# Performance work log

Hardware: AMD Instinct MI355X
Metric: run time of the kernel (lower is better)

The kernel has to match this reference:

```python
import jax, jax.numpy as jnp
import numpy as np

H, HD = 8, 32            # num_heads, head_dim
OUT = H * HD             # out_channels = 256
NUM_GRAPHS = 1


def segment_softmax(logits, seg, num_segments):
    m = jax.ops.segment_max(logits, seg, num_segments=num_segments)
    m = jnp.where(jnp.isfinite(m), m, 0.0)
    e = jnp.exp(logits - m[seg])
    s = jax.ops.segment_sum(e, seg, num_segments=num_segments)
    return e / (s[seg] + 1e-16)


def setup_inputs():
    key = jax.random.key(0)
    ks = jax.random.split(key, 16)
    N, E, IN = 30000, 600000, 128
    s = 0.05
    return {
        "x": jax.random.normal(ks[0], (N, IN), jnp.float32),
        "edge_index": jax.random.randint(ks[1], (2, E), 0, N, jnp.int32),
        "edge_attr": jax.random.normal(ks[2], (E,), jnp.float32),
        "batch": jnp.zeros((N,), jnp.int32),
        # per-head GATConv params (stacked over heads)
        "W": jax.random.normal(ks[3], (H, IN, HD), jnp.float32) * s,
        "a_src": jax.random.normal(ks[4], (H, HD), jnp.float32) * s,
        "a_dst": jax.random.normal(ks[5], (H, HD), jnp.float32) * s,
        "conv_b": jnp.zeros((H, HD), jnp.float32),
        # shared fc (used twice in forward)
        "fc_w": jax.random.normal(ks[6], (OUT, OUT), jnp.float32) * s,
        "fc_b": jnp.zeros((OUT,), jnp.float32),
        "ln_w": jnp.ones((OUT,), jnp.float32),
        "ln_b": jnp.zeros((OUT,), jnp.float32),
        "gate_w": jax.random.normal(ks[7], (1, OUT), jnp.float32) * s,
        "gate_b": jnp.zeros((1,), jnp.float32),
        "gfc_w": jax.random.normal(ks[8], (OUT, OUT), jnp.float32) * s,
        "gfc_b": jnp.zeros((OUT,), jnp.float32),
    }


def reference(x, edge_index, edge_attr, batch, W, a_src, a_dst, conv_b,
              fc_w, fc_b, ln_w, ln_b, gate_w, gate_b, gfc_w, gfc_b):
    N = x.shape[0]
    # (dropout p=0.2 is identity in eval mode)
    # --- multi-head GATConv (heads=1 each, vectorized over H); PyG default
    # add_self_loops=True; edge_dim=None so edge_attr is ignored by the conv.
    loops = jnp.arange(N, dtype=edge_index.dtype)
    src = jnp.concatenate([edge_index[0], loops])  # [Etot]
    dst = jnp.concatenate([edge_index[1], loops])
    xp = jnp.einsum('ni,hid->nhd', x, W)                    # [N,H,HD]
    alpha_src = jnp.sum(xp * a_src[None], axis=-1)          # [N,H]
    alpha_dst = jnp.sum(xp * a_dst[None], axis=-1)          # [N,H]
    logits = jax.nn.leaky_relu(alpha_src[src] + alpha_dst[dst], 0.2)  # [Etot,H]
    alpha = segment_softmax(logits, dst, N)                 # [Etot,H]
    msg = alpha[:, :, None] * xp[src]                        # [Etot,H,HD]
    out = jax.ops.segment_sum(msg, dst, num_segments=N) + conv_b[None]
    x_local = out.reshape(N, OUT)                            # concat over heads
    # --- dense re-attention / softmax fusion
    sa = jax.nn.softmax(jax.nn.leaky_relu(x_local @ fc_w.T + fc_b, 0.01), axis=-1)
    x_local = jax.nn.leaky_relu(x_local * sa, 0.2)
    x_local = x_local @ fc_w.T + fc_b
    # LayerNorm (eps=1e-5)
    mu = jnp.mean(x_local, axis=-1, keepdims=True)
    var = jnp.mean(jnp.square(x_local - mu), axis=-1, keepdims=True)
    x_local = (x_local - mu) / jnp.sqrt(var + 1e-5) * ln_w + ln_b
    # F.normalize(p=2, dim=1)
    nrm = jnp.sqrt(jnp.sum(jnp.square(x_local), axis=1, keepdims=True))
    x_local = x_local / jnp.maximum(nrm, 1e-12)
    # --- GlobalAttention pooling
    gate = (x_local @ gate_w.T + gate_b)[:, 0]               # [N]
    g = segment_softmax(gate, batch, NUM_GRAPHS)             # [N]
    x_global = jax.ops.segment_sum(g[:, None] * x_local, batch,
                                   num_segments=NUM_GRAPHS)  # [1,OUT]
    ga = jax.nn.softmax(jax.nn.relu(x_global @ gfc_w.T + gfc_b), axis=-1)
    return x_local * ga[batch]                               # [N,OUT]
```

## Files before the change

kernel.cpp:

```cpp
#include <hip/hip_runtime.h>


#define PAD 64
#define CSTR 16

typedef __attribute__((ext_vector_type(8))) short bf16x8;
typedef __attribute__((ext_vector_type(4))) float f32x4;

__device__ __forceinline__ float leaky_f(float v, float s) { return v > 0.f ? v : s * v; }
__device__ __forceinline__ unsigned short f2bf(float f) {
  unsigned int u = __float_as_uint(f);
  u += 0x7fffu + ((u >> 16) & 1u);
  return (unsigned short)(u >> 16);
}
__device__ __forceinline__ float bf2f(unsigned short u) {
  return __uint_as_float(((unsigned int)u) << 16);
}
__device__ __forceinline__ float bf_lo(unsigned int u) {
  return __uint_as_float(u << 16);
}
__device__ __forceinline__ float bf_hi(unsigned int u) {
  return __uint_as_float(u & 0xffff0000u);
}
__device__ __forceinline__ float red16_sum(float v) {
#pragma unroll
  for (int m = 1; m < 16; m <<= 1) v += __shfl_xor(v, m);
  return v;
}
__device__ __forceinline__ float red16_max(float v) {
#pragma unroll
  for (int m = 1; m < 16; m <<= 1) v = fmaxf(v, __shfl_xor(v, m));
  return v;
}

__global__ void repack_zero_kernel(const float* __restrict__ W, const float* __restrict__ fc_w,
                                   const float* __restrict__ gfc_w,
                                   unsigned short* __restrict__ Wb,
                                   unsigned short* __restrict__ fcB, float* __restrict__ gfcT,
                                   int* __restrict__ count, int n) {
  int i = blockIdx.x * 256 + threadIdx.x;
  if (i < 256 * 128) {
    int c = i >> 7, k = i & 127;
    Wb[i] = f2bf(W[((c >> 5) * 128 + k) * 32 + (c & 31)]);
  } else if (i < 256 * 128 + 256 * 256) {
    int j = i - 256 * 128;
    fcB[j] = f2bf(fc_w[j]);
  } else if (i < 256 * 128 + 2 * 256 * 256) {
    int j = i - 256 * 128 - 256 * 256;
    gfcT[j] = gfc_w[(j & 255) * 256 + (j >> 8)];
  }
  if (i < n) count[i * CSTR] = 0;
}

__device__ __forceinline__ void gemm_body_f32(
    const float* __restrict__ A, const unsigned short* __restrict__ B,
    int row0, int n_rows, int K, short As[64][72], short Bs[256][72],
    f32x4 acc[4][4]) {
  int t = threadIdx.x;
  int wave = t >> 6, lane = t & 63;
  int m16 = lane & 15, quad = lane >> 4;
  int wc = wave * 64;
  for (int k0 = 0; k0 < K; k0 += 64) {
#pragma unroll
    for (int p = 0; p < 4; ++p) {
      int e = (p * 256 + t) * 4;
      int row = e >> 6, k = e & 63;
      int ar = row0 + row; if (ar > n_rows - 1) ar = n_rows - 1;
      float4 q = *(const float4*)(A + (size_t)ar * K + k0 + k);
      unsigned int lo = (unsigned int)f2bf(q.x) | ((unsigned int)f2bf(q.y) << 16);
      unsigned int hi = (unsigned int)f2bf(q.z) | ((unsigned int)f2bf(q.w) << 16);
      *(uint2*)&As[row][k] = make_uint2(lo, hi);
    }
#pragma unroll
    for (int p = 0; p < 8; ++p) {
      int e = (p * 256 + t) * 8;
      int nn = e >> 6, k = e & 63;
      uint4 q = *(const uint4*)(B + (size_t)nn * K + k0 + k);
      *(uint4*)&Bs[nn][k] = q;
    }
    __syncthreads();
#pragma unroll
    for (int ks = 0; ks < 64; ks += 32) {
      bf16x8 af[4], bfr[4];
#pragma unroll
      for (int i = 0; i < 4; ++i)
        af[i] = *(const bf16x8*)&As[i * 16 + m16][ks + quad * 8];
#pragma unroll
      for (int j = 0; j < 4; ++j)
        bfr[j] = *(const bf16x8*)&Bs[wc + j * 16 + m16][ks + quad * 8];
#pragma unroll
      for (int i = 0; i < 4; ++i)
#pragma unroll
        for (int j = 0; j < 4; ++j)
          acc[i][j] = __builtin_amdgcn_mfma_f32_16x16x32_bf16(af[i], bfr[j], acc[i][j], 0, 0, 0);
    }
    __syncthreads();
  }
}

__global__ __launch_bounds__(256) void gemm_xp_scatter(
    const float* __restrict__ A, const unsigned short* __restrict__ B,
    const float* __restrict__ a_src, const float* __restrict__ a_dst,
    unsigned short* __restrict__ xpb, float* __restrict__ asrc,
    float* __restrict__ adst, int n_rows,
    const int* __restrict__ esrc, const int* __restrict__ edst,
    int* __restrict__ count, unsigned short* __restrict__ ssrc, int E,
    int scat_blocks) {
  __shared__ short As[64][72];
  __shared__ short Bs[256][72];
  if ((int)blockIdx.x < scat_blocks) {
    int base = ((int)blockIdx.x * 256 + threadIdx.x) * 4;
    if (base + 4 <= E) {
      int4 d4 = *(const int4*)(edst + base);
      int4 s4 = *(const int4*)(esrc + base);
      int p0 = atomicAdd(&count[d4.x * CSTR], 1);
      int p1 = atomicAdd(&count[d4.y * CSTR], 1);
      int p2 = atomicAdd(&count[d4.z * CSTR], 1);
      int p3 = atomicAdd(&count[d4.w * CSTR], 1);
      if (p0 < PAD) ssrc[(size_t)d4.x * PAD + p0] = (unsigned short)s4.x;
      if (p1 < PAD) ssrc[(size_t)d4.y * PAD + p1] = (unsigned short)s4.y;
      if (p2 < PAD) ssrc[(size_t)d4.z * PAD + p2] = (unsigned short)s4.z;
      if (p3 < PAD) ssrc[(size_t)d4.w * PAD + p3] = (unsigned short)s4.w;
    } else {
      for (int i = base; i < E; ++i) {
        int d = edst[i];
        int p = atomicAdd(&count[d * CSTR], 1);
        if (p < PAD) ssrc[(size_t)d * PAD + p] = (unsigned short)esrc[i];
      }
    }
    return;
  }
  int t = threadIdx.x;
  int wave = t >> 6, lane = t & 63;
  int m16 = lane & 15, quad = lane >> 4;
  int wc = wave * 64;
  int row0 = ((int)blockIdx.x - scat_blocks) * 64;
  f32x4 acc[4][4];
#pragma unroll
  for (int i = 0; i < 4; ++i)
#pragma unroll
    for (int j = 0; j < 4; ++j) acc[i][j] = (f32x4){0.f, 0.f, 0.f, 0.f};
  gemm_body_f32(A, B, row0, n_rows, 128, As, Bs, acc);

  float av[4], bd[4];
#pragma unroll
  for (int j = 0; j < 4; ++j) {
    int c = wc + j * 16 + m16;
    av[j] = a_src[c];
    bd[j] = a_dst[c];
  }
#pragma unroll
  for (int i = 0; i < 4; ++i)
#pragma unroll
    for (int v = 0; v < 4; ++v) {
      int r = row0 + i * 16 + quad * 4 + v;
      if (r < n_rows) {
#pragma unroll
        for (int j = 0; j < 4; ++j)
          xpb[(size_t)r * 256 + wc + j * 16 + m16] = f2bf(acc[i][j][v]);
      }
      float s0 = acc[i][0][v] * av[0] + acc[i][1][v] * av[1];
      float s1 = acc[i][2][v] * av[2] + acc[i][3][v] * av[3];
      float d0 = acc[i][0][v] * bd[0] + acc[i][1][v] * bd[1];
      float d1 = acc[i][2][v] * bd[2] + acc[i][3][v] * bd[3];
      s0 = red16_sum(s0); s1 = red16_sum(s1);
      d0 = red16_sum(d0); d1 = red16_sum(d1);
      if (m16 == 0 && r < n_rows) {
        asrc[(size_t)r * 8 + 2 * wave] = s0;
        asrc[(size_t)r * 8 + 2 * wave + 1] = s1;
        adst[(size_t)r * 8 + 2 * wave] = d0;
        adst[(size_t)r * 8 + 2 * wave + 1] = d1;
      }
    }
}

__global__ __launch_bounds__(256) void agg_kernel(
    const unsigned short* __restrict__ xpb, const float* __restrict__ asrc,
    const float* __restrict__ adst, const int* __restrict__ count,
    const unsigned short* __restrict__ ssrc, const float* __restrict__ conv_b,
    unsigned short* __restrict__ xlocb, int n_nodes) {
  int t = threadIdx.x;
  int lane = t & 63;
  int hl = lane & 31;
  int half = lane >> 5;
  int wv = t >> 6;
  int n = blockIdx.x * 8 + wv * 2 + half;
  bool active = n < n_nodes;
  int nn = active ? n : 0;
  int hc = hl >> 2;
  int hp = hl & 7;
  int up = hl >> 3;
  int srcbase = (half << 5) + hc;

  float ad_p = adst[nn * 8 + hp];
  float ad_c = adst[nn * 8 + hc];

  float p = __expf(leaky_f(asrc[nn * 8 + hc] + ad_c, 0.2f));
  uint4 q = *(const uint4*)(xpb + (size_t)nn * 256 + hl * 8);
  float acc[8];
  acc[0] = p * bf_lo(q.x); acc[1] = p * bf_hi(q.x);
  acc[2] = p * bf_lo(q.y); acc[3] = p * bf_hi(q.y);
  acc[4] = p * bf_lo(q.z); acc[5] = p * bf_hi(q.z);
  acc[6] = p * bf_lo(q.w); acc[7] = p * bf_hi(q.w);
  float ssum = p;

  int beg = nn * PAD;
  int end = beg + (active ? count[nn * CSTR] : 0);
  int j = beg;
  for (; j + 4 <= end; j += 4) {
    ushort4 s4 = *(const ushort4*)(ssrc + j);
    int svp = (up & 1) ? ((up & 2) ? s4.w : s4.y) : ((up & 2) ? s4.z : s4.x);
    float pp = __expf(leaky_f(asrc[svp * 8 + hp] + ad_p, 0.2f));
    uint4 q0 = *(const uint4*)(xpb + (size_t)s4.x * 256 + hl * 8);
    uint4 q1 = *(const uint4*)(xpb + (size_t)s4.y * 256 + hl * 8);
    uint4 q2 = *(const uint4*)(xpb + (size_t)s4.z * 256 + hl * 8);
    uint4 q3 = *(const uint4*)(xpb + (size_t)s4.w * 256 + hl * 8);
    float p0 = __shfl(pp, srcbase);
    float p1 = __shfl(pp, srcbase + 8);
    float p2 = __shfl(pp, srcbase + 16);
    float p3 = __shfl(pp, srcbase + 24);
    acc[0] += p0 * bf_lo(q0.x); acc[1] += p0 * bf_hi(q0.x);
    acc[2] += p0 * bf_lo(q0.y); acc[3] += p0 * bf_hi(q0.y);
    acc[4] += p0 * bf_lo(q0.z); acc[5] += p0 * bf_hi(q0.z);
    acc[6] += p0 * bf_lo(q0.w); acc[7] += p0 * bf_hi(q0.w);
    acc[0] += p1 * bf_lo(q1.x); acc[1] += p1 * bf_hi(q1.x);
    acc[2] += p1 * bf_lo(q1.y); acc[3] += p1 * bf_hi(q1.y);
    acc[4] += p1 * bf_lo(q1.z); acc[5] += p1 * bf_hi(q1.z);
    acc[6] += p1 * bf_lo(q1.w); acc[7] += p1 * bf_hi(q1.w);
    acc[0] += p2 * bf_lo(q2.x); acc[1] += p2 * bf_hi(q2.x);
    acc[2] += p2 * bf_lo(q2.y); acc[3] += p2 * bf_hi(q2.y);
    acc[4] += p2 * bf_lo(q2.z); acc[5] += p2 * bf_hi(q2.z);
    acc[6] += p2 * bf_lo(q2.w); acc[7] += p2 * bf_hi(q2.w);
    acc[0] += p3 * bf_lo(q3.x); acc[1] += p3 * bf_hi(q3.x);
    acc[2] += p3 * bf_lo(q3.y); acc[3] += p3 * bf_hi(q3.y);
    acc[4] += p3 * bf_lo(q3.z); acc[5] += p3 * bf_hi(q3.z);
    acc[6] += p3 * bf_lo(q3.w); acc[7] += p3 * bf_hi(q3.w);
    ssum += p0 + p1 + p2 + p3;
  }
  for (; j < end; ++j) {
    int sv = ssrc[j];
    float p1 = __expf(leaky_f(asrc[sv * 8 + hc] + ad_c, 0.2f));
    uint4 q1 = *(const uint4*)(xpb + (size_t)sv * 256 + hl * 8);
    acc[0] += p1 * bf_lo(q1.x); acc[1] += p1 * bf_hi(q1.x);
    acc[2] += p1 * bf_lo(q1.y); acc[3] += p1 * bf_hi(q1.y);
    acc[4] += p1 * bf_lo(q1.z); acc[5] += p1 * bf_hi(q1.z);
    acc[6] += p1 * bf_lo(q1.w); acc[7] += p1 * bf_hi(q1.w);
    ssum += p1;
  }
  if (!active) return;
  float inv = 1.f / (ssum + 1e-16f);
  float4 b0 = *(const float4*)(conv_b + hl * 8);
  float4 b1 = *(const float4*)(conv_b + hl * 8 + 4);
  unsigned int w0 = (unsigned int)f2bf(acc[0] * inv + b0.x) |
                    ((unsigned int)f2bf(acc[1] * inv + b0.y) << 16);
  unsigned int w1 = (unsigned int)f2bf(acc[2] * inv + b0.z) |
                    ((unsigned int)f2bf(acc[3] * inv + b0.w) << 16);
  unsigned int w2 = (unsigned int)f2bf(acc[4] * inv + b1.x) |
                    ((unsigned int)f2bf(acc[5] * inv + b1.y) << 16);
  unsigned int w3 = (unsigned int)f2bf(acc[6] * inv + b1.z) |
                    ((unsigned int)f2bf(acc[7] * inv + b1.w) << 16);
  *(uint4*)(xlocb + (size_t)n * 256 + hl * 8) = make_uint4(w0, w1, w2, w3);
}

__global__ __launch_bounds__(256) void gemm_sm_ln(
    const unsigned short* __restrict__ A, const unsigned short* __restrict__ B,
    const float* __restrict__ bias, const float* __restrict__ ln_w,
    const float* __restrict__ ln_b, const float* __restrict__ gate_w,
    const float* __restrict__ gate_b, unsigned short* __restrict__ Cout,
    float* __restrict__ pooled, float* __restrict__ pooledS, int n_rows) {
  __shared__ short X2[64][264];
  __shared__ short Bs[256][72];
  __shared__ float red[4][64];
  __shared__ float rowv[64];
  __shared__ float eg[64];
  int t = threadIdx.x;
  int wave = t >> 6, lane = t & 63;
  int m16 = lane & 15, quad = lane >> 4;
  int wc = wave * 64;
  int row0 = blockIdx.x * 64;

#pragma unroll
  for (int p = 0; p < 8; ++p) {
    int e = (p * 256 + t) * 8;
    int row = e >> 8, col = e & 255;
    int ar = row0 + row; if (ar > n_rows - 1) ar = n_rows - 1;
    uint4 qv = *(const uint4*)(A + (size_t)ar * 256 + col);
    *(uint4*)&X2[row][col] = qv;
  }

  f32x4 acc[4][4];
#pragma unroll
  for (int i = 0; i < 4; ++i)
#pragma unroll
    for (int j = 0; j < 4; ++j) acc[i][j] = (f32x4){0.f, 0.f, 0.f, 0.f};

  for (int k0 = 0; k0 < 256; k0 += 64) {
#pragma unroll
    for (int p = 0; p < 8; ++p) {
      int e = (p * 256 + t) * 8;
      int nn = e >> 6, k = e & 63;
      uint4 qv = *(const uint4*)(B + (size_t)nn * 256 + k0 + k);
      *(uint4*)&Bs[nn][k] = qv;
    }
    __syncthreads();
#pragma unroll
    for (int ks = 0; ks < 64; ks += 32) {
      bf16x8 af[4], bfr[4];
#pragma unroll
      for (int i = 0; i < 4; ++i)
        af[i] = *(const bf16x8*)&X2[i * 16 + m16][k0 + ks + quad * 8];
#pragma unroll
      for (int j = 0; j < 4; ++j)
        bfr[j] = *(const bf16x8*)&Bs[wc + j * 16 + m16][ks + quad * 8];
#pragma unroll
      for (int i = 0; i < 4; ++i)
#pragma unroll
        for (int j = 0; j < 4; ++j)
          acc[i][j] = __builtin_amdgcn_mfma_f32_16x16x32_bf16(af[i], bfr[j], acc[i][j], 0, 0, 0);
    }
    __syncthreads();
  }

  float bvv[4];
#pragma unroll
  for (int j = 0; j < 4; ++j) bvv[j] = bias[wc + j * 16 + m16];
#pragma unroll
  for (int i = 0; i < 4; ++i)
#pragma unroll
    for (int j = 0; j < 4; ++j)
#pragma unroll
      for (int v = 0; v < 4; ++v)
        acc[i][j][v] = leaky_f(acc[i][j][v] + bvv[j], 0.01f);

  float M[4][4];
#pragma unroll
  for (int i = 0; i < 4; ++i)
#pragma unroll
    for (int v = 0; v < 4; ++v) {
      float m = fmaxf(fmaxf(acc[i][0][v], acc[i][1][v]), fmaxf(acc[i][2][v], acc[i][3][v]));
      M[i][v] = red16_max(m);
    }
  if (m16 == 0)
#pragma unroll
    for (int i = 0; i < 4; ++i)
#pragma unroll
      for (int v = 0; v < 4; ++v) red[wave][i * 16 + quad * 4 + v] = M[i][v];
  __syncthreads();
  if (t < 64) rowv[t] = fmaxf(fmaxf(red[0][t], red[1][t]), fmaxf(red[2][t], red[3][t]));
  __syncthreads();
#pragma unroll
  for (int i = 0; i < 4; ++i)
#pragma unroll
    for (int v = 0; v < 4; ++v) M[i][v] = rowv[i * 16 + quad * 4 + v];
  __syncthreads();

  float S[4][4];
#pragma unroll
  for (int i = 0; i < 4; ++i)
#pragma unroll
    for (int v = 0; v < 4; ++v) {
#pragma unroll
      for (int j = 0; j < 4; ++j) acc[i][j][v] = __expf(acc[i][j][v] - M[i][v]);
      float s = acc[i][0][v] + acc[i][1][v] + acc[i][2][v] + acc[i][3][v];
      S[i][v] = red16_sum(s);
    }
  if (m16 == 0)
#pragma unroll
    for (int i = 0; i < 4; ++i)
#pragma unroll
      for (int v = 0; v < 4; ++v) red[wave][i * 16 + quad * 4 + v] = S[i][v];
  __syncthreads();
  if (t < 64) rowv[t] = red[0][t] + red[1][t] + red[2][t] + red[3][t];
  __syncthreads();

#pragma unroll
  for (int i = 0; i < 4; ++i)
#pragma unroll
    for (int v = 0; v < 4; ++v) {
      int rl = i * 16 + quad * 4 + v;
      float inv = 1.f / rowv[rl];
#pragma unroll
      for (int j = 0; j < 4; ++j) {
        int c = wc + j * 16 + m16;
        float xv = bf2f((unsigned short)X2[rl][c]);
        X2[rl][c] = (short)f2bf(leaky_f(xv * acc[i][j][v] * inv, 0.2f));
      }
    }

#pragma unroll
  for (int i = 0; i < 4; ++i)
#pragma unroll
    for (int j = 0; j < 4; ++j) acc[i][j] = (f32x4){0.f, 0.f, 0.f, 0.f};
  for (int k0 = 0; k0 < 256; k0 += 64) {
#pragma unroll
    for (int p = 0; p < 8; ++p) {
      int e = (p * 256 + t) * 8;
      int nn = e >> 6, k = e & 63;
      uint4 qv = *(const uint4*)(B + (size_t)nn * 256 + k0 + k);
      *(uint4*)&Bs[nn][k] = qv;
    }
    __syncthreads();
#pragma unroll
    for (int ks = 0; ks < 64; ks += 32) {
      bf16x8 af[4], bfr[4];
#pragma unroll
      for (int i = 0; i < 4; ++i)
        af[i] = *(const bf16x8*)&X2[i * 16 + m16][k0 + ks + quad * 8];
#pragma unroll
      for (int j = 0; j < 4; ++j)
        bfr[j] = *(const bf16x8*)&Bs[wc + j * 16 + m16][ks + quad * 8];
#pragma unroll
      for (int i = 0; i < 4; ++i)
#pragma unroll
        for (int j = 0; j < 4; ++j)
          acc[i][j] = __builtin_amdgcn_mfma_f32_16x16x32_bf16(af[i], bfr[j], acc[i][j], 0, 0, 0);
    }
    __syncthreads();
  }

  float lw[4], lb[4], gw[4];
#pragma unroll
  for (int j = 0; j < 4; ++j) {
    int c = wc + j * 16 + m16;
    bvv[j] = bias[c]; lw[j] = ln_w[c]; lb[j] = ln_b[c]; gw[j] = gate_w[c];
  }
#pragma unroll
  for (int i = 0; i < 4; ++i)
#pragma unroll
    for (int j = 0; j < 4; ++j)
#pragma unroll
      for (int v = 0; v < 4; ++v) acc[i][j][v] += bvv[j];

  float MU[4][4];
#pragma unroll
  for (int i = 0; i < 4; ++i)
#pragma unroll
    for (int v = 0; v < 4; ++v)
      MU[i][v] = red16_sum(acc[i][0][v] + acc[i][1][v] + acc[i][2][v] + acc[i][3][v]);
  if (m16 == 0)
#pragma unroll
    for (int i = 0; i < 4; ++i)
#pragma unroll
      for (int v = 0; v < 4; ++v) red[wave][i * 16 + quad * 4 + v] = MU[i][v];
  __syncthreads();
  if (t < 64) rowv[t] = (red[0][t] + red[1][t] + red[2][t] + red[3][t]) * (1.f / 256.f);
  __syncthreads();
#pragma unroll
  for (int i = 0; i < 4; ++i)
#pragma unroll
    for (int v = 0; v < 4; ++v) MU[i][v] = rowv[i * 16 + quad * 4 + v];
  __syncthreads();
#pragma unroll
  for (int i = 0; i < 4; ++i)
#pragma unroll
    for (int j = 0; j < 4; ++j)
#pragma unroll
      for (int v = 0; v < 4; ++v) acc[i][j][v] -= MU[i][v];

  float RS[4][4];
#pragma unroll
  for (int i = 0; i < 4; ++i)
#pragma unroll
    for (int v = 0; v < 4; ++v) {
      float qq = acc[i][0][v] * acc[i][0][v] + acc[i][1][v] * acc[i][1][v] +
                 acc[i][2][v] * acc[i][2][v] + acc[i][3][v] * acc[i][3][v];
      RS[i][v] = red16_sum(qq);
    }
  if (m16 == 0)
#pragma unroll
    for (int i = 0; i < 4; ++i)
#pragma unroll
      for (int v = 0; v < 4; ++v) red[wave][i * 16 + quad * 4 + v] = RS[i][v];
  __syncthreads();
  if (t < 64)
    rowv[t] = rsqrtf((red[0][t] + red[1][t] + red[2][t] + red[3][t]) * (1.f / 256.f) + 1e-5f);
  __syncthreads();
#pragma unroll
  for (int i = 0; i < 4; ++i)
#pragma unroll
    for (int v = 0; v < 4; ++v) RS[i][v] = rowv[i * 16 + quad * 4 + v];
  __syncthreads();
#pragma unroll
  for (int i = 0; i < 4; ++i)
#pragma unroll
    for (int j = 0; j < 4; ++j)
#pragma unroll
      for (int v = 0; v < 4; ++v)
        acc[i][j][v] = acc[i][j][v] * RS[i][v] * lw[j] + lb[j];

  float NV[4][4];
#pragma unroll
  for (int i = 0; i < 4; ++i)
#pragma unroll
    for (int v = 0; v < 4; ++v) {
      float qq = acc[i][0][v] * acc[i][0][v] + acc[i][1][v] * acc[i][1][v] +
                 acc[i][2][v] * acc[i][2][v] + acc[i][3][v] * acc[i][3][v];
      NV[i][v] = red16_sum(qq);
    }
  if (m16 == 0)
#pragma unroll
    for (int i = 0; i < 4; ++i)
#pragma unroll
      for (int v = 0; v < 4; ++v) red[wave][i * 16 + quad * 4 + v] = NV[i][v];
  __syncthreads();
  if (t < 64)
    rowv[t] = 1.f / fmaxf(sqrtf(red[0][t] + red[1][t] + red[2][t] + red[3][t]), 1e-12f);
  __syncthreads();
#pragma unroll
  for (int i = 0; i < 4; ++i)
#pragma unroll
    for (int v = 0; v < 4; ++v) NV[i][v] = rowv[i * 16 + quad * 4 + v];
  __syncthreads();
#pragma unroll
  for (int i = 0; i < 4; ++i)
#pragma unroll
    for (int j = 0; j < 4; ++j)
#pragma unroll
      for (int v = 0; v < 4; ++v) acc[i][j][v] *= NV[i][v];

  float GP[4][4];
#pragma unroll
  for (int i = 0; i < 4; ++i)
#pragma unroll
    for (int v = 0; v < 4; ++v) {
      float g = acc[i][0][v] * gw[0] + acc[i][1][v] * gw[1] +
                acc[i][2][v] * gw[2] + acc[i][3][v] * gw[3];
      GP[i][v] = red16_sum(g);
    }
  if (m16 == 0)
#pragma unroll
    for (int i = 0; i < 4; ++i)
#pragma unroll
      for (int v = 0; v < 4; ++v) red[wave][i * 16 + quad * 4 + v] = GP[i][v];
  __syncthreads();
  if (t < 64) {
    float gp = red[0][t] + red[1][t] + red[2][t] + red[3][t];
    float e = (row0 + t < n_rows) ? __expf(gp + gate_b[0]) : 0.f;
    eg[t] = e;
#pragma unroll
    for (int m = 1; m < 64; m <<= 1) e += __shfl_xor(e, m);
    if (t == 0) pooledS[blockIdx.x] = e;
  }
  __syncthreads();

  {
    float pt[4] = {0.f, 0.f, 0.f, 0.f};
#pragma unroll
    for (int i = 0; i < 4; ++i)
#pragma unroll
      for (int v = 0; v < 4; ++v) {
        float w = eg[i * 16 + quad * 4 + v];
#pragma unroll
        for (int j = 0; j < 4; ++j) pt[j] += w * acc[i][j][v];
      }
#pragma unroll
    for (int j = 0; j < 4; ++j) {
      float sj = pt[j];
      sj += __shfl_xor(sj, 16);
      sj += __shfl_xor(sj, 32);
      if (quad == 0) pooled[(size_t)blockIdx.x * 256 + wc + j * 16 + m16] = sj;
    }
  }

#pragma unroll
  for (int i = 0; i < 4; ++i)
#pragma unroll
    for (int v = 0; v < 4; ++v) {
      int r = row0 + i * 16 + quad * 4 + v;
      if (r < n_rows) {
#pragma unroll
        for (int j = 0; j < 4; ++j)
          Cout[(size_t)r * 256 + wc + j * 16 + m16] = f2bf(acc[i][j][v]);
      }
    }
}

__global__ __launch_bounds__(1024) void finalize_gfc(
    const float* __restrict__ pooled, const float* __restrict__ pooledS, int nb,
    const float* __restrict__ gfcT, const float* __restrict__ gfc_b,
    float* __restrict__ ga) {
  __shared__ float sm[1024];
  __shared__ float xs[256];
  __shared__ float av[256];
  int t = threadIdx.x, c = t & 255, part = t >> 8;
  float s = 0.f;
  for (int b = t; b < nb; b += 1024) s += pooledS[b];
  sm[t] = s;
  __syncthreads();
  for (int st = 512; st > 0; st >>= 1) {
    if (t < st) sm[t] += sm[t + st];
    __syncthreads();
  }
  float S = sm[0];
  __syncthreads();
  float xc = 0.f;
#pragma unroll 4
  for (int b = part; b < nb; b += 4) xc += pooled[(size_t)b * 256 + c];
  sm[t] = xc;
  __syncthreads();
  if (part == 0) xs[c] = (sm[c] + sm[c + 256] + sm[c + 512] + sm[c + 768]) / (S + 1e-16f);
  __syncthreads();
  float a = 0.f;
  for (int i = part * 64; i < part * 64 + 64; ++i) a += xs[i] * gfcT[i * 256 + c];
  sm[t] = a;
  __syncthreads();
  if (part == 0)
    av[c] = fmaxf(sm[c] + sm[c + 256] + sm[c + 512] + sm[c + 768] + gfc_b[c], 0.f);
  __syncthreads();
  sm[t] = (t < 256) ? av[t] : -1e30f;
  __syncthreads();
  for (int st = 512; st > 0; st >>= 1) {
    if (t < st) sm[t] = fmaxf(sm[t], sm[t + st]);
    __syncthreads();
  }
  float m = sm[0];
  __syncthreads();
  if (part == 0) av[c] = __expf(av[c] - m);
  __syncthreads();
  sm[t] = (t < 256) ? av[t] : 0.f;
  __syncthreads();
  for (int st = 512; st > 0; st >>= 1) {
    if (t < st) sm[t] += sm[t + st];
    __syncthreads();
  }
  if (part == 0) ga[c] = av[c] / sm[0];
}

__global__ void out_kernel(const ushort4* __restrict__ xlb4, const float4* __restrict__ ga4,
                           float4* __restrict__ out4, int total4) {
  int i = blockIdx.x * 256 + threadIdx.x;
  if (i >= total4) return;
  ushort4 q = xlb4[i];
  float4 g = ga4[i & 63];
  float4 v;
  v.x = bf2f(q.x) * g.x; v.y = bf2f(q.y) * g.y;
  v.z = bf2f(q.z) * g.z; v.w = bf2f(q.w) * g.w;
  out4[i] = v;
}

extern "C" void kernel_launch(void* const* d_in, const int* in_sizes, int n_in,
                              void* d_out, int out_size, void* d_ws, size_t ws_size,
                              hipStream_t stream) {
  const float* x      = (const float*)d_in[0];
  const int* edge_idx = (const int*)d_in[1];
  const float* W      = (const float*)d_in[4];
  const float* a_src  = (const float*)d_in[5];
  const float* a_dst  = (const float*)d_in[6];
  const float* conv_b = (const float*)d_in[7];
  const float* fc_w   = (const float*)d_in[8];
  const float* fc_b   = (const float*)d_in[9];
  const float* ln_w   = (const float*)d_in[10];
  const float* ln_b   = (const float*)d_in[11];
  const float* gate_w = (const float*)d_in[12];
  const float* gate_b = (const float*)d_in[13];
  const float* gfc_w  = (const float*)d_in[14];
  const float* gfc_b  = (const float*)d_in[15];
  (void)n_in; (void)out_size; (void)ws_size;

  int N = in_sizes[0] / 128;
  int E = in_sizes[1] / 2;
  const int* src = edge_idx;
  const int* dst = edge_idx + E;

  char* p = (char*)d_ws;
  auto alloc = [&](size_t bytes) -> char* {
    char* r = p;
    p += (bytes + 255) & ~(size_t)255;
    return r;
  };
  int g64 = (N + 63) / 64;
  unsigned short* xlocb = (unsigned short*)alloc((size_t)N * 256 * 2);
  unsigned short* xpb  = (unsigned short*)alloc((size_t)N * 256 * 2);
  unsigned short* xlb  = (unsigned short*)alloc((size_t)N * 256 * 2);
  float* asrc  = (float*)alloc((size_t)N * 8 * 4);
  float* adst  = (float*)alloc((size_t)N * 8 * 4);
  unsigned short* Wb   = (unsigned short*)alloc(256 * 128 * 2);
  unsigned short* fcB  = (unsigned short*)alloc(256 * 256 * 2);
  float* gfcT  = (float*)alloc(256 * 256 * 4);
  int*   count = (int*)alloc((size_t)N * CSTR * 4);
  unsigned short* ssrc = (unsigned short*)alloc((size_t)N * PAD * 2);
  float* pooled  = (float*)alloc((size_t)g64 * 256 * 4);
  float* pooledS = (float*)alloc((size_t)g64 * 4);
  float* ga    = (float*)alloc(1024);

  int eb4 = (E + 1023) / 1024;

  repack_zero_kernel<<<(256 * 128 + 2 * 256 * 256 + 255) / 256, 256, 0, stream>>>(
      W, fc_w, gfc_w, Wb, fcB, gfcT, count, N);
  gemm_xp_scatter<<<eb4 + g64, 256, 0, stream>>>(
      x, Wb, a_src, a_dst, xpb, asrc, adst, N, src, dst, count, ssrc, E, eb4);
  agg_kernel<<<(N + 7) / 8, 256, 0, stream>>>(
      xpb, asrc, adst, count, ssrc, conv_b, xlocb, N);
  gemm_sm_ln<<<g64, 256, 0, stream>>>(xlocb, fcB, fc_b, ln_w, ln_b, gate_w,
                                      gate_b, xlb, pooled, pooledS, N);
  finalize_gfc<<<1, 1024, 0, stream>>>(pooled, pooledS, g64, gfcT, gfc_b, ga);
  out_kernel<<<(N * 64 + 255) / 256, 256, 0, stream>>>(
      (const ushort4*)xlb, (const float4*)ga, (float4*)d_out, N * 64);
}
```

Measured before the change: 242.6 us.

## Fuse aggregation into fc GEMM and merge finalize with output scaling via flag

The edge-aggregation kernel is folded into the fc/softmax/LayerNorm GEMM kernel, so each 64-row block gathers its neighbours straight into shared memory instead of writing and re-reading an intermediate bf16 buffer. The single-block gfc finalize and the elementwise output kernel become one grid-stride kernel. In it, block 0 computes the gate vector and sets a flag, and the other blocks spin on that flag before scaling. This removes two launches and one round trip of N×256 data through global memory. The trade-off is far fewer blocks for the gather phase (one per 64 rows instead of one per 8), which may hurt latency hiding. The spin-wait also relies on block 0 being scheduled.

Result: slower. 958.3 us (+295.0%).

```diff
diff --git a/kernel.cpp b/kernel.cpp
--- a/kernel.cpp
+++ b/kernel.cpp
@@ -37,7 +37,7 @@
                                    const float* __restrict__ gfc_w,
                                    unsigned short* __restrict__ Wb,
                                    unsigned short* __restrict__ fcB, float* __restrict__ gfcT,
-                                   int* __restrict__ count, int n) {
+                                   int* __restrict__ count, int* __restrict__ flag, int n) {
   int i = blockIdx.x * 256 + threadIdx.x;
   if (i < 256 * 128) {
     int c = i >> 7, k = i & 127;
@@ -50,6 +50,7 @@
     gfcT[j] = gfc_w[(j & 255) * 256 + (j >> 8)];
   }
   if (i < n) count[i * CSTR] = 0;
+  if (i == 0) flag[0] = 0;
 }
 
 __device__ __forceinline__ void gemm_body_f32(
@@ -174,96 +175,11 @@
     }
 }
 
-__global__ __launch_bounds__(256) void agg_kernel(
+__global__ __launch_bounds__(256) void agg_sm_ln(
     const unsigned short* __restrict__ xpb, const float* __restrict__ asrc,
     const float* __restrict__ adst, const int* __restrict__ count,
     const unsigned short* __restrict__ ssrc, const float* __restrict__ conv_b,
-    unsigned short* __restrict__ xlocb, int n_nodes) {
-  int t = threadIdx.x;
-  int lane = t & 63;
-  int hl = lane & 31;
-  int half = lane >> 5;
-  int wv = t >> 6;
-  int n = blockIdx.x * 8 + wv * 2 + half;
-  bool active = n < n_nodes;
-  int nn = active ? n : 0;
-  int hc = hl >> 2;
-  int hp = hl & 7;
-  int up = hl >> 3;
-  int srcbase = (half << 5) + hc;
-
-  float ad_p = adst[nn * 8 + hp];
-  float ad_c = adst[nn * 8 + hc];
-
-  float p = __expf(leaky_f(asrc[nn * 8 + hc] + ad_c, 0.2f));
-  uint4 q = *(const uint4*)(xpb + (size_t)nn * 256 + hl * 8);
-  float acc[8];
-  acc[0] = p * bf_lo(q.x); acc[1] = p * bf_hi(q.x);
-  acc[2] = p * bf_lo(q.y); acc[3] = p * bf_hi(q.y);
-  acc[4] = p * bf_lo(q.z); acc[5] = p * bf_hi(q.z);
-  acc[6] = p * bf_lo(q.w); acc[7] = p * bf_hi(q.w);
-  float ssum = p;
-
-  int beg = nn * PAD;
-  int end = beg + (active ? count[nn * CSTR] : 0);
-  int j = beg;
-  for (; j + 4 <= end; j += 4) {
-    ushort4 s4 = *(const ushort4*)(ssrc + j);
-    int svp = (up & 1) ? ((up & 2) ? s4.w : s4.y) : ((up & 2) ? s4.z : s4.x);
-    float pp = __expf(leaky_f(asrc[svp * 8 + hp] + ad_p, 0.2f));
-    uint4 q0 = *(const uint4*)(xpb + (size_t)s4.x * 256 + hl * 8);
-    uint4 q1 = *(const uint4*)(xpb + (size_t)s4.y * 256 + hl * 8);
-    uint4 q2 = *(const uint4*)(xpb + (size_t)s4.z * 256 + hl * 8);
-    uint4 q3 = *(const uint4*)(xpb + (size_t)s4.w * 256 + hl * 8);
-    float p0 = __shfl(pp, srcbase);
-    float p1 = __shfl(pp, srcbase + 8);
-    float p2 = __shfl(pp, srcbase + 16);
-    float p3 = __shfl(pp, srcbase + 24);
-    acc[0] += p0 * bf_lo(q0.x); acc[1] += p0 * bf_hi(q0.x);
-    acc[2] += p0 * bf_lo(q0.y); acc[3] += p0 * bf_hi(q0.y);
-    acc[4] += p0 * bf_lo(q0.z); acc[5] += p0 * bf_hi(q0.z);
-    acc[6] += p0 * bf_lo(q0.w); acc[7] += p0 * bf_hi(q0.w);
-    acc[0] += p1 * bf_lo(q1.x); acc[1] += p1 * bf_hi(q1.x);
-    acc[2] += p1 * bf_lo(q1.y); acc[3] += p1 * bf_hi(q1.y);
-    acc[4] += p1 * bf_lo(q1.z); acc[5] += p1 * bf_hi(q1.z);
-    acc[6] += p1 * bf_lo(q1.w); acc[7] += p1 * bf_hi(q1.w);
-    acc[0] += p2 * bf_lo(q2.x); acc[1] += p2 * bf_hi(q2.x);
-    acc[2] += p2 * bf_lo(q2.y); acc[3] += p2 * bf_hi(q2.y);
-    acc[4] += p2 * bf_lo(q2.z); acc[5] += p2 * bf_hi(q2.z);
-    acc[6] += p2 * bf_lo(q2.w); acc[7] += p2 * bf_hi(q2.w);
-    acc[0] += p3 * bf_lo(q3.x); acc[1] += p3 * bf_hi(q3.x);
-    acc[2] += p3 * bf_lo(q3.y); acc[3] += p3 * bf_hi(q3.y);
-    acc[4] += p3 * bf_lo(q3.z); acc[5] += p3 * bf_hi(q3.z);
-    acc[6] += p3 * bf_lo(q3.w); acc[7] += p3 * bf_hi(q3.w);
-    ssum += p0 + p1 + p2 + p3;
-  }
-  for (; j < end; ++j) {
-    int sv = ssrc[j];
-    float p1 = __expf(leaky_f(asrc[sv * 8 + hc] + ad_c, 0.2f));
-    uint4 q1 = *(const uint4*)(xpb + (size_t)sv * 256 + hl * 8);
-    acc[0] += p1 * bf_lo(q1.x); acc[1] += p1 * bf_hi(q1.x);
-    acc[2] += p1 * bf_lo(q1.y); acc[3] += p1 * bf_hi(q1.y);
-    acc[4] += p1 * bf_lo(q1.z); acc[5] += p1 * bf_hi(q1.z);
-    acc[6] += p1 * bf_lo(q1.w); acc[7] += p1 * bf_hi(q1.w);
-    ssum += p1;
-  }
-  if (!active) return;
-  float inv = 1.f / (ssum + 1e-16f);
-  float4 b0 = *(const float4*)(conv_b + hl * 8);
-  float4 b1 = *(const float4*)(conv_b + hl * 8 + 4);
-  unsigned int w0 = (unsigned int)f2bf(acc[0] * inv + b0.x) |
-                    ((unsigned int)f2bf(acc[1] * inv + b0.y) << 16);
-  unsigned int w1 = (unsigned int)f2bf(acc[2] * inv + b0.z) |
-                    ((unsigned int)f2bf(acc[3] * inv + b0.w) << 16);
-  unsigned int w2 = (unsigned int)f2bf(acc[4] * inv + b1.x) |
-                    ((unsigned int)f2bf(acc[5] * inv + b1.y) << 16);
-  unsigned int w3 = (unsigned int)f2bf(acc[6] * inv + b1.z) |
-                    ((unsigned int)f2bf(acc[7] * inv + b1.w) << 16);
-  *(uint4*)(xlocb + (size_t)n * 256 + hl * 8) = make_uint4(w0, w1, w2, w3);
-}
-
-__global__ __launch_bounds__(256) void gemm_sm_ln(
-    const unsigned short* __restrict__ A, const unsigned short* __restrict__ B,
+    const unsigned short* __restrict__ B,
     const float* __restrict__ bias, const float* __restrict__ ln_w,
     const float* __restrict__ ln_b, const float* __restrict__ gate_w,
     const float* __restrict__ gate_b, unsigned short* __restrict__ Cout,
@@ -279,14 +195,89 @@
   int wc = wave * 64;
   int row0 = blockIdx.x * 64;
 
-#pragma unroll
-  for (int p = 0; p < 8; ++p) {
-    int e = (p * 256 + t) * 8;
-    int row = e >> 8, col = e & 255;
-    int ar = row0 + row; if (ar > n_rows - 1) ar = n_rows - 1;
-    uint4 qv = *(const uint4*)(A + (size_t)ar * 256 + col);
-    *(uint4*)&X2[row][col] = qv;
-  }
+  {
+    int hl = lane & 31;
+    int half = lane >> 5;
+    int hc = hl >> 2;
+    int hp = hl & 7;
+    int up = hl >> 3;
+    int srcbase = (half << 5) + hc;
+    for (int it = 0; it < 8; ++it) {
+      int lr = wave * 16 + it * 2 + half;
+      int n = row0 + lr;
+      bool active = n < n_rows;
+      int nn = active ? n : 0;
+      float ad_p = adst[nn * 8 + hp];
+      float ad_c = adst[nn * 8 + hc];
+      float p = __expf(leaky_f(asrc[nn * 8 + hc] + ad_c, 0.2f));
+      uint4 q = *(const uint4*)(xpb + (size_t)nn * 256 + hl * 8);
+      float a8[8];
+      a8[0] = p * bf_lo(q.x); a8[1] = p * bf_hi(q.x);
+      a8[2] = p * bf_lo(q.y); a8[3] = p * bf_hi(q.y);
+      a8[4] = p * bf_lo(q.z); a8[5] = p * bf_hi(q.z);
+      a8[6] = p * bf_lo(q.w); a8[7] = p * bf_hi(q.w);
+      float ssum = p;
+      int beg = nn * PAD;
+      int end = beg + (active ? count[nn * CSTR] : 0);
+      int j = beg;
+      for (; j + 4 <= end; j += 4) {
+        ushort4 s4 = *(const ushort4*)(ssrc + j);
+        int svp = (up & 1) ? ((up & 2) ? s4.w : s4.y) : ((up & 2) ? s4.z : s4.x);
+        float pp = __expf(leaky_f(asrc[svp * 8 + hp] + ad_p, 0.2f));
+        uint4 q0 = *(const uint4*)(xpb + (size_t)s4.x * 256 + hl * 8);
+        uint4 q1 = *(const uint4*)(xpb + (size_t)s4.y * 256 + hl * 8);
+        uint4 q2 = *(const uint4*)(xpb + (size_t)s4.z * 256 + hl * 8);
+        uint4 q3 = *(const uint4*)(xpb + (size_t)s4.w * 256 + hl * 8);
+        float p0 = __shfl(pp, srcbase);
+        float p1 = __shfl(pp, srcbase + 8);
+        float p2 = __shfl(pp, srcbase + 16);
+        float p3 = __shfl(pp, srcbase + 24);
+        a8[0] += p0 * bf_lo(q0.x); a8[1] += p0 * bf_hi(q0.x);
+        a8[2] += p0 * bf_lo(q0.y); a8[3] += p0 * bf_hi(q0.y);
+        a8[4] += p0 * bf_lo(q0.z); a8[5] += p0 * bf_hi(q0.z);
+        a8[6] += p0 * bf_lo(q0.w); a8[7] += p0 * bf_hi(q0.w);
+        a8[0] += p1 * bf_lo(q1.x); a8[1] += p1 * bf_hi(q1.x);
+        a8[2] += p1 * bf_lo(q1.y); a8[3] += p1 * bf_hi(q1.y);
+        a8[4] += p1 * bf_lo(q1.z); a8[5] += p1 * bf_hi(q1.z);
+        a8[6] += p1 * bf_lo(q1.w); a8[7] += p1 * bf_hi(q1.w);
+        a8[0] += p2 * bf_lo(q2.x); a8[1] += p2 * bf_hi(q2.x);
+        a8[2] += p2 * bf_lo(q2.y); a8[3] += p2 * bf_hi(q2.y);
+        a8[4] += p2 * bf_lo(q2.z); a8[5] += p2 * bf_hi(q2.z);
+        a8[6] += p2 * bf_lo(q2.w); a8[7] += p2 * bf_hi(q2.w);
+        a8[0] += p3 * bf_lo(q3.x); a8[1] += p3 * bf_hi(q3.x);
+        a8[2] += p3 * bf_lo(q3.y); a8[3] += p3 * bf_hi(q3.y);
+        a8[4] += p3 * bf_lo(q3.z); a8[5] += p3 * bf_hi(q3.z);
+        a8[6] += p3 * bf_lo(q3.w); a8[7] += p3 * bf_hi(q3.w);
+        ssum += p0 + p1 + p2 + p3;
+      }
+      for (; j < end; ++j) {
+        int sv = ssrc[j];
+        float p1 = __expf(leaky_f(asrc[sv * 8 + hc] + ad_c, 0.2f));
+        uint4 q1 = *(const uint4*)(xpb + (size_t)sv * 256 + hl * 8);
+        a8[0] += p1 * bf_lo(q1.x); a8[1] += p1 * bf_hi(q1.x);
+        a8[2] += p1 * bf_lo(q1.y); a8[3] += p1 * bf_hi(q1.y);
+        a8[4] += p1 * bf_lo(q1.z); a8[5] += p1 * bf_hi(q1.z);
+        a8[6] += p1 * bf_lo(q1.w); a8[7] += p1 * bf_hi(q1.w);
+        ssum += p1;
+      }
+      unsigned int w0 = 0, w1 = 0, w2 = 0, w3 = 0;
+      if (active) {
+        float inv = 1.f / (ssum + 1e-16f);
+        float4 b0 = *(const float4*)(conv_b + hl * 8);
+        float4 b1 = *(const float4*)(conv_b + hl * 8 + 4);
+        w0 = (unsigned int)f2bf(a8[0] * inv + b0.x) |
+             ((unsigned int)f2bf(a8[1] * inv + b0.y) << 16);
+        w1 = (unsigned int)f2bf(a8[2] * inv + b0.z) |
+             ((unsigned int)f2bf(a8[3] * inv + b0.w) << 16);
+        w2 = (unsigned int)f2bf(a8[4] * inv + b1.x) |
+             ((unsigned int)f2bf(a8[5] * inv + b1.y) << 16);
+        w3 = (unsigned int)f2bf(a8[6] * inv + b1.z) |
+             ((unsigned int)f2bf(a8[7] * inv + b1.w) << 16);
+      }
+      *(uint4*)&X2[lr][hl * 8] = make_uint4(w0, w1, w2, w3);
+    }
+  }
+  __syncthreads();
 
   f32x4 acc[4][4];
 #pragma unroll
@@ -575,67 +566,67 @@
     }
 }
 
-__global__ __launch_bounds__(1024) void finalize_gfc(
+__global__ __launch_bounds__(256) void finalize_out(
     const float* __restrict__ pooled, const float* __restrict__ pooledS, int nb,
     const float* __restrict__ gfcT, const float* __restrict__ gfc_b,
-    float* __restrict__ ga) {
-  __shared__ float sm[1024];
+    const ushort4* __restrict__ xlb4, float4* __restrict__ out4, int total4,
+    float* __restrict__ gaBuf, int* __restrict__ flag) {
+  int t = threadIdx.x;
   __shared__ float xs[256];
-  __shared__ float av[256];
-  int t = threadIdx.x, c = t & 255, part = t >> 8;
-  float s = 0.f;
-  for (int b = t; b < nb; b += 1024) s += pooledS[b];
-  sm[t] = s;
-  __syncthreads();
-  for (int st = 512; st > 0; st >>= 1) {
-    if (t < st) sm[t] += sm[t + st];
-    __syncthreads();
-  }
-  float S = sm[0];
-  __syncthreads();
-  float xc = 0.f;
-#pragma unroll 4
-  for (int b = part; b < nb; b += 4) xc += pooled[(size_t)b * 256 + c];
-  sm[t] = xc;
-  __syncthreads();
-  if (part == 0) xs[c] = (sm[c] + sm[c + 256] + sm[c + 512] + sm[c + 768]) / (S + 1e-16f);
-  __syncthreads();
-  float a = 0.f;
-  for (int i = part * 64; i < part * 64 + 64; ++i) a += xs[i] * gfcT[i * 256 + c];
-  sm[t] = a;
-  __syncthreads();
-  if (part == 0)
-    av[c] = fmaxf(sm[c] + sm[c + 256] + sm[c + 512] + sm[c + 768] + gfc_b[c], 0.f);
-  __syncthreads();
-  sm[t] = (t < 256) ? av[t] : -1e30f;
-  __syncthreads();
-  for (int st = 512; st > 0; st >>= 1) {
-    if (t < st) sm[t] = fmaxf(sm[t], sm[t + st]);
-    __syncthreads();
-  }
-  float m = sm[0];
-  __syncthreads();
-  if (part == 0) av[c] = __expf(av[c] - m);
-  __syncthreads();
-  sm[t] = (t < 256) ? av[t] : 0.f;
-  __syncthreads();
-  for (int st = 512; st > 0; st >>= 1) {
-    if (t < st) sm[t] += sm[t + st];
-    __syncthreads();
-  }
-  if (part == 0) ga[c] = av[c] / sm[0];
-}
-
-__global__ void out_kernel(const ushort4* __restrict__ xlb4, const float4* __restrict__ ga4,
-                           float4* __restrict__ out4, int total4) {
-  int i = blockIdx.x * 256 + threadIdx.x;
-  if (i >= total4) return;
-  ushort4 q = xlb4[i];
-  float4 g = ga4[i & 63];
-  float4 v;
-  v.x = bf2f(q.x) * g.x; v.y = bf2f(q.y) * g.y;
-  v.z = bf2f(q.z) * g.z; v.w = bf2f(q.w) * g.w;
-  out4[i] = v;
+  __shared__ float red[256];
+  if (blockIdx.x == 0) {
+    float s = 0.f;
+    for (int b = t; b < nb; b += 256) s += pooledS[b];
+    red[t] = s;
+    __syncthreads();
+    for (int st = 128; st > 0; st >>= 1) {
+      if (t < st) red[t] += red[t + st];
+      __syncthreads();
+    }
+    float S = red[0];
+    __syncthreads();
+    float xc = 0.f;
+    for (int b = 0; b < nb; ++b) xc += pooled[(size_t)b * 256 + t];
+    xs[t] = xc / (S + 1e-16f);
+    __syncthreads();
+    float a = gfc_b[t];
+    for (int i = 0; i < 256; ++i) a += xs[i] * gfcT[i * 256 + t];
+    a = fmaxf(a, 0.f);
+    red[t] = a;
+    __syncthreads();
+    for (int st = 128; st > 0; st >>= 1) {
+      if (t < st) red[t] = fmaxf(red[t], red[t + st]);
+      __syncthreads();
+    }
+    float m = red[0];
+    __syncthreads();
+    float e = __expf(a - m);
+    red[t] = e;
+    __syncthreads();
+    for (int st = 128; st > 0; st >>= 1) {
+      if (t < st) red[t] += red[t + st];
+      __syncthreads();
+    }
+    gaBuf[t] = e / red[0];
+    __syncthreads();
+    __threadfence();
+    if (t == 0) __hip_atomic_store(flag, 1, __ATOMIC_RELEASE, __HIP_MEMORY_SCOPE_AGENT);
+  } else {
+    if (t == 0) {
+      while (__hip_atomic_load(flag, __ATOMIC_ACQUIRE, __HIP_MEMORY_SCOPE_AGENT) == 0) {
+      }
+    }
+    __syncthreads();
+  }
+  const float4* ga4 = (const float4*)gaBuf;
+  for (int i = blockIdx.x * 256 + t; i < total4; i += (int)gridDim.x * 256) {
+    ushort4 q = xlb4[i];
+    float4 g = ga4[i & 63];
+    float4 v;
+    v.x = bf2f(q.x) * g.x; v.y = bf2f(q.y) * g.y;
+    v.z = bf2f(q.z) * g.z; v.w = bf2f(q.w) * g.w;
+    out4[i] = v;
+  }
 }
 
 extern "C" void kernel_launch(void* const* d_in, const int* in_sizes, int n_in,
@@ -669,7 +660,6 @@
     return r;
   };
   int g64 = (N + 63) / 64;
-  unsigned short* xlocb = (unsigned short*)alloc((size_t)N * 256 * 2);
   unsigned short* xpb  = (unsigned short*)alloc((size_t)N * 256 * 2);
   unsigned short* xlb  = (unsigned short*)alloc((size_t)N * 256 * 2);
   float* asrc  = (float*)alloc((size_t)N * 8 * 4);
@@ -682,18 +672,18 @@
   float* pooled  = (float*)alloc((size_t)g64 * 256 * 4);
   float* pooledS = (float*)alloc((size_t)g64 * 4);
   float* ga    = (float*)alloc(1024);
+  int*   flag  = (int*)alloc(256);
 
   int eb4 = (E + 1023) / 1024;
 
   repack_zero_kernel<<<(256 * 128 + 2 * 256 * 256 + 255) / 256, 256, 0, stream>>>(
-      W, fc_w, gfc_w, Wb, fcB, gfcT, count, N);
+      W, fc_w, gfc_w, Wb, fcB, gfcT, count, flag, N);
   gemm_xp_scatter<<<eb4 + g64, 256, 0, stream>>>(
       x, Wb, a_src, a_dst, xpb, asrc, adst, N, src, dst, count, ssrc, E, eb4);
-  agg_kernel<<<(N + 7) / 8, 256, 0, stream>>>(
-      xpb, asrc, adst, count, ssrc, conv_b, xlocb, N);
-  gemm_sm_ln<<<g64, 256, 0, stream>>>(xlocb, fcB, fc_b, ln_w, ln_b, gate_w,
-                                      gate_b, xlb, pooled, pooledS, N);
-  finalize_gfc<<<1, 1024, 0, stream>>>(pooled, pooledS, g64, gfcT, gfc_b, ga);
-  out_kernel<<<(N * 64 + 255) / 256, 256, 0, stream>>>(
-      (const ushort4*)xlb, (const float4*)ga, (float4*)d_out, N * 64);
-}
+  agg_sm_ln<<<g64, 256, 0, stream>>>(
+      xpb, asrc, adst, count, ssrc, conv_b, fcB, fc_b, ln_w, ln_b, gate_w,
+      gate_b, xlb, pooled, pooledS, N);
+  finalize_out<<<512, 256, 0, stream>>>(
+      pooled, pooledS, g64, gfcT, gfc_b, (const ushort4*)xlb, (float4*)d_out,
+      N * 64, ga, flag);
+}
```
